# Performance work log

Hardware: AMD Instinct MI355X
Metric: run time of the kernel (lower is better)

## Reference

```python
import jax, jax.numpy as jnp
import numpy as np

N = 100000
E = 500000
F_IN = 128
HID = 64
HEADS = 4
OUT = 32
NEG_SLOPE = 0.2


def _glorot(key, shape):
    fan_in, fan_out = shape[0], shape[1]
    lim = jnp.sqrt(6.0 / (fan_in + fan_out))
    return jax.random.uniform(key, shape, jnp.float32, -lim, lim)


def setup_inputs() -> dict:
    key = jax.random.key(0)
    ks = jax.random.split(key, 20)
    x = jax.random.normal(ks[0], (N, F_IN), jnp.float32)
    edge_index = jax.random.randint(ks[1], (2, E), 0, N, jnp.int64)
    edge_attr = jax.random.uniform(ks[2], (E, 1), jnp.float32)
    d1 = HEADS * HID
    params = {
        # conv1: F_IN -> HEADS x HID
        "Wl1": _glorot(ks[3], (F_IN, d1)), "bl1": jnp.zeros((d1,), jnp.float32),
        "Wr1": _glorot(ks[4], (F_IN, d1)), "br1": jnp.zeros((d1,), jnp.float32),
        "We1": _glorot(ks[5], (1, d1)),
        "att1": _glorot(ks[6], (HEADS, HID)),
        "b1": jnp.zeros((d1,), jnp.float32),
        "Wl2": _glorot(ks[7], (d1, OUT)), "bl2": jnp.zeros((OUT,), jnp.float32),
        "Wr2": _glorot(ks[8], (d1, OUT)), "br2": jnp.zeros((OUT,), jnp.float32),
        "We2": _glorot(ks[9], (1, OUT)),
        "att2": _glorot(ks[10], (1, OUT)),
        "b2": jnp.zeros((OUT,), jnp.float32),
    }
    return {"x": x, "edge_index": edge_index, "edge_attr": edge_attr, **params}


def gatv2_conv(x, src, dst, edge_attr, Wl, bl, Wr, br, We, att, bias, heads, out_ch):
    """PyG GATv2Conv (add_self_loops=False, concat=True, share_weights=False)."""
    n = x.shape[0]
    xl = (x @ Wl + bl).reshape(n, heads, out_ch)          # source transform
    xr = (x @ Wr + br).reshape(n, heads, out_ch)          # target transform
    e = (edge_attr @ We).reshape(-1, heads, out_ch)       # [E, H, C]
    m = jax.nn.leaky_relu(xl[src] + xr[dst] + e, NEG_SLOPE)  # [E, H, C]
    alpha = jnp.einsum('ehc,hc->eh', m, att)              # [E, H]
    # softmax over edges sharing the same destination node
    amax = jax.ops.segment_max(alpha, dst, num_segments=n)
    ealpha = jnp.exp(alpha - amax[dst])
    denom = jax.ops.segment_sum(ealpha, dst, num_segments=n)
    alpha = ealpha / (denom[dst] + 1e-16)
    out = jax.ops.segment_sum(xl[src] * alpha[:, :, None], dst, num_segments=n)
    return out.reshape(n, heads * out_ch) + bias


def reference(x, edge_index, edge_attr, Wl1, bl1, Wr1, br1, We1, att1, b1,
              Wl2, bl2, Wr2, br2, We2, att2, b2):
    src, dst = edge_index[0], edge_index[1]
    h = gatv2_conv(x, src, dst, edge_attr, Wl1, bl1, Wr1, br1, We1, att1, b1, HEADS, HID)
    h = jax.nn.relu(h)  # dropout is identity at inference
    out = gatv2_conv(h, src, dst, edge_attr, Wl2, bl2, Wr2, br2, We2, att2, b2, 1, OUT)
    return out
```

## Files before the change

### kernel.cpp

```cpp
#include <hip/hip_runtime.h>
#include <cstddef>
#include <cstdint>

#define F_IN 128
#define D1   256
#define HEADS 4
#define HID   64
#define OUT_C 32
#define NEG   0.2f

typedef unsigned short ushort_t;
typedef __attribute__((ext_vector_type(8))) short short8;
typedef __attribute__((ext_vector_type(4))) float f32x4;
typedef __attribute__((ext_vector_type(4))) unsigned short ushort4v;

__device__ __forceinline__ float bu2f(ushort_t u) {
  return __uint_as_float(((unsigned)u) << 16);
}
__device__ __forceinline__ ushort_t f2bu(float f) {
  unsigned u = __float_as_uint(f);
  return (ushort_t)((u + 0x7FFF + ((u >> 16) & 1)) >> 16);
}

__global__ void prep_k(const float* __restrict__ Wl1, const float* __restrict__ Wr1,
                       const float* __restrict__ bl1, const float* __restrict__ br1,
                       ushort_t* __restrict__ Bt1, float* __restrict__ bias1c,
                       const float* __restrict__ Wl2, const float* __restrict__ Wr2,
                       const float* __restrict__ bl2, const float* __restrict__ br2,
                       ushort_t* __restrict__ Bt2, float* __restrict__ bias2c) {
  int b = blockIdx.x;
  if (b < 256) {
    int i = b * 256 + threadIdx.x;
    int nn = i >> 7, k = i & 127;
    float v = (nn < D1) ? Wl1[(size_t)k * D1 + nn] : Wr1[(size_t)k * D1 + (nn - D1)];
    Bt1[(size_t)nn * F_IN + k] = f2bu(v);
    if (k == 0) bias1c[nn] = (nn < D1) ? bl1[nn] : br1[nn - D1];
  } else {
    int i = (b - 256) * 256 + threadIdx.x;
    int nn = i >> 8, k = i & 255;
    float v = (nn < OUT_C) ? Wl2[(size_t)k * OUT_C + nn] : Wr2[(size_t)k * OUT_C + (nn - OUT_C)];
    Bt2[(size_t)nn * D1 + k] = f2bu(v);
    if (k == 0) bias2c[nn] = (nn < OUT_C) ? bl2[nn] : br2[nn - OUT_C];
  }
}

template <int WM, int WN, int BK, bool CVT>
__global__ void mfma_gemm(const void* __restrict__ Av, const ushort_t* __restrict__ Bt,
                          const float* __restrict__ biasc, ushort_t* __restrict__ C,
                          int M, int N, int K) {
  constexpr int BM = WM * 64, BN = WN * 64;
  constexpr int LD = BK + 8;
  constexpr int CPR = BK / 8;
  __shared__ ushort_t As[BM][LD];
  __shared__ ushort_t Bs[BN][LD];
  const int tid = threadIdx.x;
  const int wave = tid >> 6, lane = tid & 63;
  const int wm = wave % WM, wn = wave / WM;
  const int quad = lane >> 4, l16 = lane & 15;
  const int m0 = blockIdx.y * BM, n0 = blockIdx.x * BN;
  const int nth = WM * WN * 64;
  f32x4 acc[4][4] = {};
  for (int k0 = 0; k0 < K; k0 += BK) {
    for (int i = tid; i < BM * CPR; i += nth) {
      int r = i / CPR, ch = i % CPR;
      int gr = m0 + r;
      if (CVT) {
        const float* A32 = (const float*)Av;
        f32x4 v0 = {}, v1 = {};
        if (gr < M) {
          const float* p = A32 + (size_t)gr * K + k0 + ch * 8;
          v0 = *(const f32x4*)p;
          v1 = *(const f32x4*)(p + 4);
        }
        short8 o;
        o[0] = (short)f2bu(v0[0]); o[1] = (short)f2bu(v0[1]);
        o[2] = (short)f2bu(v0[2]); o[3] = (short)f2bu(v0[3]);
        o[4] = (short)f2bu(v1[0]); o[5] = (short)f2bu(v1[1]);
        o[6] = (short)f2bu(v1[2]); o[7] = (short)f2bu(v1[3]);
        *(short8*)(&As[r][ch * 8]) = o;
      } else {
        const ushort_t* A16 = (const ushort_t*)Av;
        short8 v = {};
        if (gr < M) v = *(const short8*)(A16 + (size_t)gr * K + k0 + ch * 8);
        *(short8*)(&As[r][ch * 8]) = v;
      }
    }
    for (int i = tid; i < BN * CPR; i += nth) {
      int r = i / CPR, ch = i % CPR;
      short8 v = {};
      if (n0 + r < N) v = *(const short8*)(Bt + (size_t)(n0 + r) * K + k0 + ch * 8);
      *(short8*)(&Bs[r][ch * 8]) = v;
    }
    __syncthreads();
#pragma unroll
    for (int ks = 0; ks < BK; ks += 32) {
      short8 af[4], bfr[4];
#pragma unroll
      for (int mi = 0; mi < 4; ++mi)
        af[mi] = *(const short8*)(&As[wm * 64 + mi * 16 + l16][ks + quad * 8]);
#pragma unroll
      for (int ni = 0; ni < 4; ++ni)
        bfr[ni] = *(const short8*)(&Bs[wn * 64 + ni * 16 + l16][ks + quad * 8]);
#pragma unroll
      for (int mi = 0; mi < 4; ++mi)
#pragma unroll
        for (int ni = 0; ni < 4; ++ni)
          acc[mi][ni] = __builtin_amdgcn_mfma_f32_16x16x32_bf16(af[mi], bfr[ni],
                                                                acc[mi][ni], 0, 0, 0);
    }
    __syncthreads();
  }
#pragma unroll
  for (int mi = 0; mi < 4; ++mi) {
#pragma unroll
    for (int r = 0; r < 4; ++r) {
      int grow = m0 + wm * 64 + mi * 16 + quad * 4 + r;
      if (grow >= M) continue;
#pragma unroll
      for (int ni = 0; ni < 4; ++ni) {
        int gcol = n0 + wn * 64 + ni * 16 + l16;
        C[(size_t)grow * N + gcol] = f2bu(acc[mi][ni][r] + biasc[gcol]);
      }
    }
  }
}

__global__ void hist_k(const int* __restrict__ dst, int* __restrict__ deg, int e) {
  int i = blockIdx.x * blockDim.x + threadIdx.x;
  if (i < e) atomicAdd(&deg[dst[i]], 1);
}

__global__ void scan_block_k(const int* __restrict__ deg, int* __restrict__ row_ptr,
                             int* __restrict__ bsum, int n) {
  __shared__ int s[1024];
  int i = blockIdx.x * 1024 + threadIdx.x;
  int v = (i < n) ? deg[i] : 0;
  s[threadIdx.x] = v;
  __syncthreads();
  for (int off = 1; off < 1024; off <<= 1) {
    int t = (threadIdx.x >= off) ? s[threadIdx.x - off] : 0;
    __syncthreads();
    s[threadIdx.x] += t;
    __syncthreads();
  }
  if (i < n) row_ptr[i + 1] = s[threadIdx.x];
  if (threadIdx.x == 1023) bsum[blockIdx.x] = s[1023];
}

__global__ void scan_bsum_k(int* __restrict__ bsum, int nb) {
  __shared__ int s[128];
  int v = (threadIdx.x < nb) ? bsum[threadIdx.x] : 0;
  s[threadIdx.x] = v;
  __syncthreads();
  for (int off = 1; off < 128; off <<= 1) {
    int t = (threadIdx.x >= off) ? s[threadIdx.x - off] : 0;
    __syncthreads();
    s[threadIdx.x] += t;
    __syncthreads();
  }
  if (threadIdx.x < nb) bsum[threadIdx.x] = s[threadIdx.x] - v;
}

__global__ void add_off_k(int* __restrict__ row_ptr, int* __restrict__ cursor,
                          const int* __restrict__ bsum, int n) {
  int i = blockIdx.x * blockDim.x + threadIdx.x;
  if (i == 0) { row_ptr[0] = 0; cursor[0] = 0; }
  if (i < n) {
    int v = row_ptr[i + 1] + bsum[i >> 10];
    row_ptr[i + 1] = v;
    if (i + 1 < n) cursor[i + 1] = v;
  }
}

__global__ void fill_k(const int* __restrict__ src, const int* __restrict__ dst,
                       const float* __restrict__ eattr, int* __restrict__ cursor,
                       int2* __restrict__ csr, int e) {
  int i = blockIdx.x * blockDim.x + threadIdx.x;
  if (i >= e) return;
  int p = atomicAdd(&cursor[dst[i]], 1);
  csr[p] = make_int2(src[i], __float_as_int(eattr[i]));
}

__global__ void gat1_k(const int* __restrict__ row_ptr, const int2* __restrict__ csr,
                       const ushort_t* __restrict__ C1,
                       const float* __restrict__ We, const float* __restrict__ att,
                       const float* __restrict__ bias, ushort_t* __restrict__ h1, int n) {
  int node = (int)(((size_t)blockIdx.x * blockDim.x + threadIdx.x) >> 6);
  int lane = threadIdx.x & 63;
  if (node >= n) return;
  int cb = lane * 4;
  ushort4v xr4 = *(const ushort4v*)(C1 + (size_t)node * 512 + 256 + cb);
  float xrr[4], Wev[4], attv[4], acc[4] = {0.f, 0.f, 0.f, 0.f};
  float esum = 0.f;
#pragma unroll
  for (int j = 0; j < 4; ++j) {
    xrr[j] = bu2f(xr4[j]);
    Wev[j] = We[cb + j];
    attv[j] = att[cb + j];
  }
  int p = row_ptr[node], p1 = row_ptr[node + 1];
  int pl = p1 - 1;
  for (int pb = p; pb < p1; pb += 4) {
    int2 ee[4];
#pragma unroll
    for (int u = 0; u < 4; ++u) {
      int q = pb + u;
      ee[u] = csr[q < p1 ? q : pl];
    }
    ushort4v xl4[4];
#pragma unroll
    for (int u = 0; u < 4; ++u)
      xl4[u] = *(const ushort4v*)(C1 + (size_t)ee[u].x * 512 + cb);
    float xv[4][4], v[4];
#pragma unroll
    for (int u = 0; u < 4; ++u) {
      float wgt = __int_as_float(ee[u].y);
      v[u] = 0.f;
#pragma unroll
      for (int j = 0; j < 4; ++j) {
        xv[u][j] = bu2f(xl4[u][j]);
        float m = xv[u][j] + xrr[j] + wgt * Wev[j];
        m = fmaxf(m, NEG * m);
        v[u] += m * attv[j];
      }
    }
#pragma unroll
    for (int u = 0; u < 4; ++u) {
      v[u] += __shfl_xor(v[u], 1, 64);
      v[u] += __shfl_xor(v[u], 2, 64);
      v[u] += __shfl_xor(v[u], 4, 64);
      v[u] += __shfl_xor(v[u], 8, 64);
    }
#pragma unroll
    for (int u = 0; u < 4; ++u) {
      float eh = (pb + u < p1) ? __expf(v[u]) : 0.f;
      esum += eh;
#pragma unroll
      for (int j = 0; j < 4; ++j) acc[j] += eh * xv[u][j];
    }
  }
  float inv = 1.f / (esum + 1e-16f);
  ushort4v o;
#pragma unroll
  for (int j = 0; j < 4; ++j) {
    float t = acc[j] * inv + bias[cb + j];
    o[j] = f2bu(t > 0.f ? t : 0.f);
  }
  *(ushort4v*)(h1 + (size_t)node * D1 + cb) = o;
}

__global__ void gat2_k(const int* __restrict__ row_ptr, const int2* __restrict__ csr,
                       const ushort_t* __restrict__ C2,
                       const float* __restrict__ We, const float* __restrict__ att,
                       const float* __restrict__ bias, float* __restrict__ out, int n) {
  int node = (int)(((size_t)blockIdx.x * blockDim.x + threadIdx.x) >> 6);
  int lane = threadIdx.x & 63;
  if (node >= n) return;
  int g = lane >> 3;
  int cb = (lane & 7) * 4;
  ushort4v xr4 = *(const ushort4v*)(C2 + (size_t)node * 64 + 32 + cb);
  float xrr[4], Wev[4], attv[4], acc[4] = {0.f, 0.f, 0.f, 0.f};
  float esum = 0.f;
#pragma unroll
  for (int j = 0; j < 4; ++j) {
    xrr[j] = bu2f(xr4[j]);
    Wev[j] = We[cb + j];
    attv[j] = att[cb + j];
  }
  int p = row_ptr[node], p1 = row_ptr[node + 1];
  int pl = p1 - 1;
  for (int pb = p; pb < p1; pb += 8) {
    int q = pb + g;
    int2 ed = csr[q < p1 ? q : pl];
    float wgt = __int_as_float(ed.y);
    ushort4v xl4 = *(const ushort4v*)(C2 + (size_t)ed.x * 64 + cb);
    float xv[4], v = 0.f;
#pragma unroll
    for (int j = 0; j < 4; ++j) {
      xv[j] = bu2f(xl4[j]);
      float m = xv[j] + xrr[j] + wgt * Wev[j];
      m = fmaxf(m, NEG * m);
      v += m * attv[j];
    }
    v += __shfl_xor(v, 1, 64);
    v += __shfl_xor(v, 2, 64);
    v += __shfl_xor(v, 4, 64);
    float eh = (q < p1) ? __expf(v) : 0.f;
    esum += eh;
#pragma unroll
    for (int j = 0; j < 4; ++j) acc[j] += eh * xv[j];
  }
  esum += __shfl_xor(esum, 8, 64);
  esum += __shfl_xor(esum, 16, 64);
  esum += __shfl_xor(esum, 32, 64);
#pragma unroll
  for (int j = 0; j < 4; ++j) {
    acc[j] += __shfl_xor(acc[j], 8, 64);
    acc[j] += __shfl_xor(acc[j], 16, 64);
    acc[j] += __shfl_xor(acc[j], 32, 64);
  }
  if (lane < 8) {
    float inv = 1.f / (esum + 1e-16f);
    f32x4 ov;
#pragma unroll
    for (int j = 0; j < 4; ++j) ov[j] = acc[j] * inv + bias[cb + j];
    *(f32x4*)(out + (size_t)node * OUT_C + cb) = ov;
  }
}

extern "C" void kernel_launch(void* const* d_in, const int* in_sizes, int n_in,
                              void* d_out, int out_size, void* d_ws, size_t ws_size,
                              hipStream_t stream) {
  const float* x     = (const float*)d_in[0];
  const int*   eidx  = (const int*)d_in[1];
  const float* eattr = (const float*)d_in[2];
  const float* Wl1 = (const float*)d_in[3];
  const float* bl1 = (const float*)d_in[4];
  const float* Wr1 = (const float*)d_in[5];
  const float* br1 = (const float*)d_in[6];
  const float* We1 = (const float*)d_in[7];
  const float* att1 = (const float*)d_in[8];
  const float* b1  = (const float*)d_in[9];
  const float* Wl2 = (const float*)d_in[10];
  const float* bl2 = (const float*)d_in[11];
  const float* Wr2 = (const float*)d_in[12];
  const float* br2 = (const float*)d_in[13];
  const float* We2 = (const float*)d_in[14];
  const float* att2 = (const float*)d_in[15];
  const float* b2  = (const float*)d_in[16];

  const int n = in_sizes[0] / F_IN;
  const int e = in_sizes[2];
  const int* src = eidx;
  const int* dst = eidx + e;
  float* out = (float*)d_out;

  char* w = (char*)d_ws;
  ushort_t* C1   = (ushort_t*)w;  w += (size_t)n * 512 * 2;
  ushort_t* h1b  = (ushort_t*)w;  w += (size_t)n * D1 * 2;
  ushort_t* C2   = (ushort_t*)w;  w += (size_t)n * 64 * 2;
  ushort_t* Bt1  = (ushort_t*)w;  w += 512 * F_IN * 2;
  ushort_t* Bt2  = (ushort_t*)w;  w += 64 * D1 * 2;
  float* bias1c  = (float*)w;     w += 512 * 4;
  float* bias2c  = (float*)w;     w += 64 * 4;
  int2*  csr     = (int2*)w;      w += (size_t)e * 8;
  int*   row_ptr = (int*)w;       w += ((size_t)n + 1) * 4;
  int*   cursor  = (int*)w;       w += (size_t)n * 4;
  int*   bsum    = (int*)w;       w += 512;
  int*   deg = cursor;

  dim3 blk(256);
  const int nb = (n + 1023) / 1024;

  prep_k<<<320, blk, 0, stream>>>(Wl1, Wr1, bl1, br1, Bt1, bias1c,
                                  Wl2, Wr2, bl2, br2, Bt2, bias2c);

  hipMemsetAsync(deg, 0, (size_t)n * sizeof(int), stream);
  hist_k<<<(e + 255) / 256, blk, 0, stream>>>(dst, deg, e);
  scan_block_k<<<nb, 1024, 0, stream>>>(deg, row_ptr, bsum, n);
  scan_bsum_k<<<1, 128, 0, stream>>>(bsum, nb);
  add_off_k<<<(n + 255) / 256, blk, 0, stream>>>(row_ptr, cursor, bsum, n);
  fill_k<<<(e + 255) / 256, blk, 0, stream>>>(src, dst, eattr, cursor, csr, e);

  mfma_gemm<2, 2, 64, true><<<dim3(4, (n + 127) / 128), blk, 0, stream>>>(
      x, Bt1, bias1c, C1, n, 512, F_IN);
  gat1_k<<<(n + 3) / 4, blk, 0, stream>>>(row_ptr, csr, C1, We1, att1, b1, h1b, n);

  mfma_gemm<2, 1, 64, false><<<dim3(1, (n + 127) / 128), dim3(128), 0, stream>>>(
      h1b, Bt2, bias2c, C2, n, 64, D1);
  gat2_k<<<(n + 3) / 4, blk, 0, stream>>>(row_ptr, csr, C2, We2, att2, b2, out, n);
}
```

Measured before the change: 368.6 us.

## Specialize first-layer GEMM to load x once and sweep all output panels

Replaces the generic tiled GEMM for the first projection with a dedicated kernel. Each block converts a 128-row tile of x to bf16 in shared memory once, then loops over four 128-column panels of the combined Wl/Wr weights. B fragments are read straight from global memory and shared memory is not staged over K. The old grid re-read and re-converted the fp32 x tile for each of 4 column blocks; the new kernel reads it once, at the cost of uncached B loads from global and more serial work per block.

```diff
diff --git a/kernel.cpp b/kernel.cpp
--- a/kernel.cpp
+++ b/kernel.cpp
@@ -41,6 +41,76 @@
     float v = (nn < OUT_C) ? Wl2[(size_t)k * OUT_C + nn] : Wr2[(size_t)k * OUT_C + (nn - OUT_C)];
     Bt2[(size_t)nn * D1 + k] = f2bu(v);
     if (k == 0) bias2c[nn] = (nn < OUT_C) ? bl2[nn] : br2[nn - OUT_C];
+  }
+}
+
+__global__ __launch_bounds__(256, 4) void gemm1_k(
+    const float* __restrict__ x, const ushort_t* __restrict__ Bt,
+    const float* __restrict__ biasc, ushort_t* __restrict__ C, int M) {
+  constexpr int LD = F_IN + 8;
+  __shared__ ushort_t As[128][LD];
+  const int tid = threadIdx.x;
+  const int wave = tid >> 6, lane = tid & 63;
+  const int wm = wave & 1, wn = wave >> 1;
+  const int quad = lane >> 4, l16 = lane & 15;
+  const int m0 = blockIdx.x * 128;
+#pragma unroll
+  for (int it = 0; it < 8; ++it) {
+    int i = it * 256 + tid;
+    int r = i >> 4, ch = i & 15;
+    int gr = m0 + r;
+    f32x4 v0 = {}, v1 = {};
+    if (gr < M) {
+      const float* p = x + (size_t)gr * F_IN + ch * 8;
+      v0 = *(const f32x4*)p;
+      v1 = *(const f32x4*)(p + 4);
+    }
+    short8 o;
+    o[0] = (short)f2bu(v0[0]); o[1] = (short)f2bu(v0[1]);
+    o[2] = (short)f2bu(v0[2]); o[3] = (short)f2bu(v0[3]);
+    o[4] = (short)f2bu(v1[0]); o[5] = (short)f2bu(v1[1]);
+    o[6] = (short)f2bu(v1[2]); o[7] = (short)f2bu(v1[3]);
+    *(short8*)(&As[r][ch * 8]) = o;
+  }
+  __syncthreads();
+  const ushort_t* Bw = Bt + (size_t)(wn * 64 + l16) * F_IN + quad * 8;
+#pragma unroll
+  for (int panel = 0; panel < 4; ++panel) {
+    const ushort_t* Bp = Bw + (size_t)panel * 128 * F_IN;
+    const int nbase = panel * 128 + wn * 64;
+    float bv[4];
+#pragma unroll
+    for (int ni = 0; ni < 4; ++ni) bv[ni] = biasc[nbase + ni * 16 + l16];
+    f32x4 acc[4][4] = {};
+#pragma unroll
+    for (int ks = 0; ks < 4; ++ks) {
+      short8 af[4], bfr[4];
+#pragma unroll
+      for (int ni = 0; ni < 4; ++ni)
+        bfr[ni] = *(const short8*)(Bp + (size_t)ni * 16 * F_IN + ks * 32);
+#pragma unroll
+      for (int mi = 0; mi < 4; ++mi)
+        af[mi] = *(const short8*)(&As[wm * 64 + mi * 16 + l16][ks * 32 + quad * 8]);
+#pragma unroll
+      for (int mi = 0; mi < 4; ++mi)
+#pragma unroll
+        for (int ni = 0; ni < 4; ++ni)
+          acc[mi][ni] = __builtin_amdgcn_mfma_f32_16x16x32_bf16(af[mi], bfr[ni],
+                                                                acc[mi][ni], 0, 0, 0);
+    }
+#pragma unroll
+    for (int mi = 0; mi < 4; ++mi) {
+#pragma unroll
+      for (int r = 0; r < 4; ++r) {
+        int grow = m0 + wm * 64 + mi * 16 + quad * 4 + r;
+        if (grow >= M) continue;
+#pragma unroll
+        for (int ni = 0; ni < 4; ++ni) {
+          int gcol = nbase + ni * 16 + l16;
+          C[(size_t)grow * 512 + gcol] = f2bu(acc[mi][ni][r] + bv[ni]);
+        }
+      }
+    }
   }
 }
 
@@ -362,8 +432,7 @@
   add_off_k<<<(n + 255) / 256, blk, 0, stream>>>(row_ptr, cursor, bsum, n);
   fill_k<<<(e + 255) / 256, blk, 0, stream>>>(src, dst, eattr, cursor, csr, e);
 
-  mfma_gemm<2, 2, 64, true><<<dim3(4, (n + 127) / 128), blk, 0, stream>>>(
-      x, Bt1, bias1c, C1, n, 512, F_IN);
+  gemm1_k<<<(n + 127) / 128, blk, 0, stream>>>(x, Bt1, bias1c, C1, n);
   gat1_k<<<(n + 3) / 4, blk, 0, stream>>>(row_ptr, csr, C1, We1, att1, b1, h1b, n);
 
   mfma_gemm<2, 1, 64, false><<<dim3(1, (n + 127) / 128), dim3(128), 0, stream>>>(
```

Measured after the change: 394.5 us. +7.0%, slower.
